# Kernel tuning notes

Hardware: AMD Instinct MI355X
Metric: run time of the kernel (lower is better)

The kernel has to match this reference:

```python
import jax, jax.numpy as jnp
import numpy as np


def setup_inputs() -> dict:
    key = jax.random.key(0)
    ks = jax.random.split(key, 8)
    B, C, H, W = 4, 512, 64, 64
    C8 = C // 8
    return {
        "x": jax.random.normal(ks[0], (B, C, H, W), dtype=jnp.float32),
        "Wq": jax.random.normal(ks[1], (C8, C), dtype=jnp.float32) * 0.02,
        "bq": jax.random.normal(ks[2], (C8,), dtype=jnp.float32) * 0.02,
        "Wk": jax.random.normal(ks[3], (C8, C), dtype=jnp.float32) * 0.02,
        "bk": jax.random.normal(ks[4], (C8,), dtype=jnp.float32) * 0.02,
        "Wv": jax.random.normal(ks[5], (C, C), dtype=jnp.float32) * 0.02,
        "bv": jax.random.normal(ks[6], (C,), dtype=jnp.float32) * 0.02,
        "gamma": jax.random.normal(ks[7], (1,), dtype=jnp.float32),
    }


def reference(x, Wq, bq, Wk, bk, Wv, bv, gamma):
    B, C, H, W = x.shape
    N = H * W
    xf = x.reshape(B, C, N)  # 1x1 conv == per-position matmul over channels
    q = jnp.einsum('oc,bcn->bno', Wq, xf) + bq  # B, N, C//8  (proj_query^T)
    k = jnp.einsum('oc,bcn->bon', Wk, xf) + bk[None, :, None]  # B, C//8, N
    v = jnp.einsum('oc,bcn->bon', Wv, xf) + bv[None, :, None]  # B, C, N
    energy = jnp.einsum('bno,bom->bnm', q, k)  # B, N, N
    attention = jax.nn.softmax(energy, axis=-1)
    # out = bmm(proj_value, attention^T): out[:, :, n] = sum_m v[:, :, m] * att[n, m]
    out = jnp.einsum('bcm,bnm->bcn', v, attention).reshape(B, C, H, W)
    return gamma[0] * out + x
```

## Files before the change

kernel.cpp:

```cpp
#include <hip/hip_runtime.h>
#include <stdint.h>


typedef unsigned short u16;
typedef unsigned char u8;
typedef __attribute__((ext_vector_type(8))) short short8;
typedef __attribute__((ext_vector_type(4))) float f32x4;
typedef __attribute__((ext_vector_type(16))) float f32x16;
typedef __attribute__((ext_vector_type(4))) int i32x4;
typedef __attribute__((ext_vector_type(8))) int i32x8;

#define ASYNC16(gp, lp)                                                        \
  __builtin_amdgcn_global_load_lds(                                            \
      (__attribute__((address_space(1))) void*)(void*)(gp),                    \
      (__attribute__((address_space(3))) void*)(lp), 16, 0, 0)

#define WAIT_VM0 0x0F70
#define WAIT_VM2 0x0F72
#define WAIT_VM4 0x0F74
#define WAIT_VM8 0x0F78

#define EXP_SHIFT 5.0f
#define EXP_CAP 57000.0f

__device__ __forceinline__ u16 f2bf(float f) {
  uint32_t u = __float_as_uint(f);
  u += 0x7FFFu + ((u >> 16) & 1u);
  return (u16)(u >> 16);
}

__device__ __forceinline__ u8 f2fp8(float f) {
  f = fminf(fmaxf(f, -440.f), 440.f);
  int r = __builtin_amdgcn_cvt_pk_fp8_f32(f, f, 0, false);
  return (u8)(r & 0xFF);
}

__global__ __launch_bounds__(256) void k_transpose(const float* __restrict__ x,
                                                   u16* __restrict__ xT) {
  __shared__ float tile[32][33];
  const int b = blockIdx.z;
  const int nb = blockIdx.x * 32;
  const int cb = blockIdx.y * 32;
  const int t = threadIdx.x;
  {
    const int nl = t & 31, c0 = t >> 5;
    const float* xp = x + ((size_t)b * 512 + cb) * 4096 + nb;
#pragma unroll
    for (int i = 0; i < 4; ++i) {
      const int cl = c0 + i * 8;
      tile[cl][nl] = xp[(size_t)cl * 4096 + nl];
    }
  }
  __syncthreads();
  {
    const int cl = t & 31, n0 = t >> 5;
    u16* xtp = xT + ((size_t)b * 4096 + nb) * 512 + cb;
#pragma unroll
    for (int i = 0; i < 4; ++i) {
      const int nl = n0 + i * 8;
      xtp[(size_t)nl * 512 + cl] = f2bf(tile[cl][nl]);
    }
  }
}

__global__ __launch_bounds__(256) void k_wcast(const float* __restrict__ Wq,
                                               const float* __restrict__ Wk,
                                               const float* __restrict__ Wv,
                                               u16* __restrict__ wqk,
                                               u16* __restrict__ wv) {
  const int idx = blockIdx.x * 256 + threadIdx.x;
  if (idx < 128 * 512) {
    const int r = idx >> 9, c = idx & 511;
    const float f = (r < 64) ? Wq[r * 512 + c] : Wk[(r - 64) * 512 + c];
    wqk[idx] = f2bf(f);
  } else {
    const int j = idx - 128 * 512;
    if (j < 512 * 512) wv[j] = f2bf(Wv[j]);
  }
}

__device__ __forceinline__ void gemm_bt_tile(const u16* __restrict__ A,
                                             const u16* __restrict__ B,
                                             const int K, const int rowA0,
                                             const int colB0, u16* smem,
                                             f32x4 acc[4][4]) {
  const int t = threadIdx.x;
  const int lane = t & 63, wave = t >> 6;
  const int quad = lane >> 4, l15 = lane & 15;
  const int wr = wave >> 1, wc = wave & 1;
  u16* As = smem;
  u16* Bs = smem + 8192;
  const f32x4 zero = {0.f, 0.f, 0.f, 0.f};
#pragma unroll
  for (int i = 0; i < 4; ++i)
#pragma unroll
    for (int j = 0; j < 4; ++j) acc[i][j] = zero;

  const int srow = t >> 3;
  const int c8 = (lane & 7) ^ (lane >> 3);
  const u16* ga = A + (size_t)(rowA0 + srow) * K + c8 * 8;
  const u16* gb = B + (size_t)(colB0 + srow) * K + c8 * 8;
  char* la = (char*)As + wave * 1024;
  char* lb = (char*)Bs + wave * 1024;
  const size_t rK32 = (size_t)32 * K;

  const int sw0 = (quad) ^ (l15 & 7);
  const int sw1 = (4 + quad) ^ (l15 & 7);

  for (int k0 = 0; k0 < K; k0 += 64) {
    ASYNC16(ga + k0, la);
    ASYNC16(ga + k0 + rK32, la + 4096);
    ASYNC16(ga + k0 + 2 * rK32, la + 8192);
    ASYNC16(ga + k0 + 3 * rK32, la + 12288);
    ASYNC16(gb + k0, lb);
    ASYNC16(gb + k0 + rK32, lb + 4096);
    ASYNC16(gb + k0 + 2 * rK32, lb + 8192);
    ASYNC16(gb + k0 + 3 * rK32, lb + 12288);
    __syncthreads();
#pragma unroll
    for (int s = 0; s < 2; ++s) {
      const int sw = s ? sw1 : sw0;
      short8 a[4], b[4];
#pragma unroll
      for (int i = 0; i < 4; ++i)
        a[i] = *(const short8*)(As + (wr * 64 + i * 16 + l15) * 64 + sw * 8);
#pragma unroll
      for (int j = 0; j < 4; ++j)
        b[j] = *(const short8*)(Bs + (wc * 64 + j * 16 + l15) * 64 + sw * 8);
#pragma unroll
      for (int i = 0; i < 4; ++i)
#pragma unroll
        for (int j = 0; j < 4; ++j)
          acc[i][j] = __builtin_amdgcn_mfma_f32_16x16x32_bf16(a[i], b[j],
                                                              acc[i][j], 0, 0, 0);
    }
    __syncthreads();
  }
}

__global__ __launch_bounds__(256) void k_proj_qk(const u16* __restrict__ xT,
                                                 const u16* __restrict__ wqk,
                                                 const float* __restrict__ bq,
                                                 const float* __restrict__ bk,
                                                 u16* __restrict__ q,
                                                 u16* __restrict__ kT) {
  __shared__ u16 smem[16384];
  const int b = blockIdx.z;
  const int rowA0 = blockIdx.x * 128;
  f32x4 acc[4][4];
  gemm_bt_tile(xT + (size_t)b * 4096 * 512, wqk, 512, rowA0, 0, smem, acc);
  const int t = threadIdx.x, lane = t & 63, wave = t >> 6;
  const int quad = lane >> 4, l15 = lane & 15;
  const int wr = wave >> 1, wc = wave & 1;
#pragma unroll
  for (int j = 0; j < 4; ++j) {
    const int col = wc * 64 + j * 16 + l15;
    const float bias = (col < 64) ? bq[col] : bk[col - 64];
#pragma unroll
    for (int i = 0; i < 4; ++i) {
#pragma unroll
      for (int r = 0; r < 4; ++r) {
        const int row = rowA0 + wr * 64 + i * 16 + quad * 4 + r;
        const float val = acc[i][j][r] + bias;
        if (col < 64)
          q[((size_t)b * 4096 + row) * 64 + col] = f2bf(val);
        else
          kT[((size_t)b * 4096 + row) * 64 + (col - 64)] = f2bf(val);
      }
    }
  }
}

__global__ __launch_bounds__(256) void k_proj_v(const u16* __restrict__ wv,
                                                const u16* __restrict__ xT,
                                                const float* __restrict__ bv,
                                                u8* __restrict__ v8) {
  __shared__ u16 smem[16384];
  const int b = blockIdx.z;
  const int rowA0 = blockIdx.x * 128;
  const int colB0 = blockIdx.y * 128;
  f32x4 acc[4][4];
  gemm_bt_tile(wv, xT + (size_t)b * 4096 * 512, 512, rowA0, colB0, smem, acc);
  const int t = threadIdx.x, lane = t & 63, wave = t >> 6;
  const int quad = lane >> 4, l15 = lane & 15;
  const int wr = wave >> 1, wc = wave & 1;
#pragma unroll
  for (int i = 0; i < 4; ++i) {
#pragma unroll
    for (int r = 0; r < 4; ++r) {
      const int row = rowA0 + wr * 64 + i * 16 + quad * 4 + r;
      const float bias = bv[row];
#pragma unroll
      for (int j = 0; j < 4; ++j) {
        const int col = colB0 + wc * 64 + j * 16 + l15;
        v8[((size_t)b * 512 + row) * 4096 + col] = f2fp8(acc[i][j][r] + bias);
      }
    }
  }
}

__global__ __launch_bounds__(256, 4) void k_attn(const u16* __restrict__ q,
                                                 const u16* __restrict__ kT,
                                                 u8* __restrict__ E8,
                                                 float* __restrict__ lpart) {
  __shared__ u16 qs[4][16 * 64];
  __shared__ u16 ks[2][128 * 64];

  const int t = threadIdx.x;
  const int l = t & 63;
  const int w = t >> 6;
  const int quad = l >> 4, l15 = l & 15;
  const int c8 = (l & 7) ^ (l >> 3);
  const int r8 = l >> 3;

  const int row0 = blockIdx.x * 64 + w * 16;
  const int mpart = blockIdx.y;
  const int b = blockIdx.z;
  const int m_base = mpart * 1024;

  const u16* qg = q + ((size_t)b * 4096 + row0) * 64 + (size_t)r8 * 64 + c8 * 8;
  const u16* kg = kT + ((size_t)b * 4096 + m_base + w * 32) * 64 +
                  (size_t)r8 * 64 + c8 * 8;

  char* qls = (char*)qs + w * 2048;
  char* kls0 = (char*)ks[0] + w * 4096;
  char* kls1 = (char*)ks[1] + w * 4096;

  ASYNC16(qg, qls);
  ASYNC16(qg + 512, qls + 1024);
#pragma unroll
  for (int i = 0; i < 4; ++i) ASYNC16(kg + i * 512, kls0 + i * 1024);
#pragma unroll
  for (int i = 0; i < 4; ++i) ASYNC16(kg + 8192 + i * 512, kls1 + i * 1024);

  __builtin_amdgcn_s_waitcnt(WAIT_VM8);

  const int sw0 = quad ^ (l15 & 7);
  const int sw1 = (4 + quad) ^ (l15 & 7);
  const u16* qsw = qs[w];
  const short8 af0 = *(const short8*)(qsw + l15 * 64 + sw0 * 8);
  const short8 af1 = *(const short8*)(qsw + l15 * 64 + sw1 * 8);

  float lsum = 0.f;
  u8* Ep = E8 + ((size_t)b * 4096 + row0 + l15) * 4096 + m_base + quad * 4;
  const f32x4 zero = {0.f, 0.f, 0.f, 0.f};

  for (int it = 0; it < 8; ++it) {
    if (it < 7)
      __builtin_amdgcn_s_waitcnt(WAIT_VM4);
    else
      __builtin_amdgcn_s_waitcnt(WAIT_VM0);
    __builtin_amdgcn_s_barrier();
    asm volatile("" ::: "memory");

    const u16* kb = ks[it & 1];
    f32x4 acc[8];
#pragma unroll
    for (int j = 0; j < 8; ++j) acc[j] = zero;
    __builtin_amdgcn_s_setprio(1);
#pragma unroll
    for (int j = 0; j < 8; ++j)
      acc[j] = __builtin_amdgcn_mfma_f32_16x16x32_bf16(
          *(const short8*)(kb + (j * 16 + l15) * 64 + sw0 * 8), af0, acc[j], 0, 0, 0);
#pragma unroll
    for (int j = 0; j < 8; ++j)
      acc[j] = __builtin_amdgcn_mfma_f32_16x16x32_bf16(
          *(const short8*)(kb + (j * 16 + l15) * 64 + sw1 * 8), af1, acc[j], 0, 0, 0);
    __builtin_amdgcn_s_setprio(0);
#pragma unroll
    for (int j = 0; j < 8; ++j) {
      const float e0 = fminf(__expf(acc[j][0] - EXP_SHIFT), EXP_CAP);
      const float e1 = fminf(__expf(acc[j][1] - EXP_SHIFT), EXP_CAP);
      const float e2 = fminf(__expf(acc[j][2] - EXP_SHIFT), EXP_CAP);
      const float e3 = fminf(__expf(acc[j][3] - EXP_SHIFT), EXP_CAP);
      lsum += (e0 + e1) + (e2 + e3);
      int pk = __builtin_amdgcn_cvt_pk_bf8_f32(e0, e1, 0, false);
      pk = __builtin_amdgcn_cvt_pk_bf8_f32(e2, e3, pk, true);
      *(int*)(Ep + it * 128 + j * 16) = pk;
    }

    asm volatile("" ::: "memory");
    __builtin_amdgcn_s_barrier();
    if (it < 6) {
      char* dst = (it & 1) ? kls1 : kls0;
      const u16* src = kg + (size_t)(it + 2) * 8192;
#pragma unroll
      for (int i = 0; i < 4; ++i) ASYNC16(src + i * 512, dst + i * 1024);
    }
  }

  lsum += __shfl_xor(lsum, 16);
  lsum += __shfl_xor(lsum, 32);
  if (l < 16)
    lpart[(size_t)mpart * 16384 + (size_t)b * 4096 + row0 + l] = lsum;
}

__global__ __launch_bounds__(256) void k_lsum(const float* __restrict__ lp,
                                              float* __restrict__ ilg) {
  const int i = blockIdx.x * 256 + threadIdx.x;
  ilg[i] = 1.0f / (lp[i] + lp[16384 + i] + lp[32768 + i] + lp[49152 + i]);
}

__global__ __launch_bounds__(512, 4) void k_pv(const u8* __restrict__ v8,
                                               const u8* __restrict__ E8,
                                               const float* __restrict__ ilg,
                                               const float* __restrict__ x,
                                               const float* __restrict__ gamma,
                                               float* __restrict__ out) {
  __shared__ u8 As[4][8192];
  __shared__ u8 Bs[4][8192];
  const int bid = blockIdx.x;
  const int xcd = bid & 7;
  const int slot = bid >> 3;
  const int c_idx = slot >> 4;
  const int group = xcd * 16 + (slot & 15);
  const int b = group >> 5;
  const int n_idx = group & 31;
  const int rowA0 = c_idx * 128;
  const int colB0 = n_idx * 128;

  const u8* Ag = v8 + (size_t)b * 512 * 4096;
  const u8* Bg = E8 + (size_t)b * 4096 * 4096;

  const int t = threadIdx.x;
  const int l = t & 63, w = t >> 6;
  const int wr = w >> 2, wc = w & 3;
  const int l31 = l & 31, h = l >> 5;

  const int srow = w * 16 + (l >> 2);
  const int ca = l & 3;
  const int fs = (srow >> 1) & 3;
  const u8* gA = Ag + (size_t)(rowA0 + srow) * 4096 + (ca ^ fs) * 16;
  const u8* gB = Bg + (size_t)(colB0 + srow) * 4096 + (ca ^ fs) * 16;

#define STAGE_PV(bi, k0)                                                       \
  do {                                                                         \
    ASYNC16(gA + (k0), (char*)As[bi] + w * 1024);                              \
    ASYNC16(gB + (k0), (char*)Bs[bi] + w * 1024);                              \
  } while (0)

  int rowA[2], sA1[2], sA2[2];
#pragma unroll
  for (int i = 0; i < 2; ++i) {
    rowA[i] = wr * 64 + i * 32 + l31;
    const int fa = (rowA[i] >> 1) & 3;
    sA1[i] = (2 * h) ^ fa;
    sA2[i] = (2 * h + 1) ^ fa;
  }
  const int rowB = wc * 32 + l31;
  const int fb = (rowB >> 1) & 3;
  const int sB1 = (2 * h) ^ fb;
  const int sB2 = (2 * h + 1) ^ fb;

  f32x16 acc[2];
#pragma unroll
  for (int i = 0; i < 2; ++i)
#pragma unroll
    for (int r = 0; r < 16; ++r) acc[i][r] = 0.f;

  STAGE_PV(0, 0);
  STAGE_PV(1, 64);
  STAGE_PV(2, 128);

  for (int it = 0; it < 64; ++it) {
    if (it < 62)
      __builtin_amdgcn_s_waitcnt(WAIT_VM4);
    else if (it == 62)
      __builtin_amdgcn_s_waitcnt(WAIT_VM2);
    else
      __builtin_amdgcn_s_waitcnt(WAIT_VM0);
    asm volatile("" ::: "memory");
    __builtin_amdgcn_s_barrier();
    asm volatile("" ::: "memory");
    if (it + 3 < 64) STAGE_PV((it + 3) & 3, (it + 3) * 64);

    const u8* Asb = As[it & 3];
    const u8* Bsb = Bs[it & 3];
    i32x8 a[2], bb;
#pragma unroll
    for (int i = 0; i < 2; ++i) {
      const u8* pa = Asb + rowA[i] * 64;
      const i32x4 lo = *(const i32x4*)(pa + sA1[i] * 16);
      const i32x4 hi = *(const i32x4*)(pa + sA2[i] * 16);
      a[i][0] = lo[0]; a[i][1] = lo[1]; a[i][2] = lo[2]; a[i][3] = lo[3];
      a[i][4] = hi[0]; a[i][5] = hi[1]; a[i][6] = hi[2]; a[i][7] = hi[3];
    }
    {
      const u8* pb = Bsb + rowB * 64;
      const i32x4 blo = *(const i32x4*)(pb + sB1 * 16);
      const i32x4 bhi = *(const i32x4*)(pb + sB2 * 16);
      bb[0] = blo[0]; bb[1] = blo[1]; bb[2] = blo[2]; bb[3] = blo[3];
      bb[4] = bhi[0]; bb[5] = bhi[1]; bb[6] = bhi[2]; bb[7] = bhi[3];
    }
    __builtin_amdgcn_s_setprio(1);
#pragma unroll
    for (int i = 0; i < 2; ++i)
      acc[i] = __builtin_amdgcn_mfma_scale_f32_32x32x64_f8f6f4(
          a[i], bb, acc[i], 0 , 1 , 0, 0x7F, 0, 0x7F);
    __builtin_amdgcn_s_setprio(0);
    asm volatile("" ::: "memory");
  }
#undef STAGE_PV

  const float g = gamma[0];
  const int col = colB0 + wc * 32 + l31;
  const float gil = g * ilg[(size_t)b * 4096 + col];
#pragma unroll
  for (int i = 0; i < 2; ++i) {
#pragma unroll
    for (int r = 0; r < 16; ++r) {
      const int rloc = (r & 3) + 8 * (r >> 2) + 4 * h;
      const int row = rowA0 + wr * 64 + i * 32 + rloc;
      const size_t idx = ((size_t)b * 512 + row) * 4096 + col;
      out[idx] = gil * acc[i][r] + x[idx];
    }
  }
}

extern "C" void kernel_launch(void* const* d_in, const int* in_sizes, int n_in,
                              void* d_out, int out_size, void* d_ws,
                              size_t ws_size, hipStream_t stream) {
  const float* x = (const float*)d_in[0];
  const float* Wq = (const float*)d_in[1];
  const float* bq = (const float*)d_in[2];
  const float* Wk = (const float*)d_in[3];
  const float* bk = (const float*)d_in[4];
  const float* Wv = (const float*)d_in[5];
  const float* bv = (const float*)d_in[6];
  const float* gamma = (const float*)d_in[7];
  float* out = (float*)d_out;

  char* ws = (char*)d_ws;
  u16* xT = (u16*)(ws);
  u16* wqk = (u16*)(ws + 16777216);
  u16* wv = (u16*)(ws + 16908288);
  u16* qb = (u16*)(ws + 17432576);
  u16* ktb = (u16*)(ws + 19529728);
  u8* v8 = (u8*)(ws + 21626880);
  u8* E8 = (u8*)(ws + 30015488);
  float* lpart = (float*)(ws + 97124352);
  float* ilg = (float*)(ws + 97386496);

  k_transpose<<<dim3(128, 16, 4), 256, 0, stream>>>(x, xT);
  k_wcast<<<dim3(1280), 256, 0, stream>>>(Wq, Wk, Wv, wqk, wv);
  k_proj_qk<<<dim3(32, 1, 4), 256, 0, stream>>>(xT, wqk, bq, bk, qb, ktb);
  k_proj_v<<<dim3(4, 32, 4), 256, 0, stream>>>(wv, xT, bv, v8);
  k_attn<<<dim3(64, 4, 4), 256, 0, stream>>>(qb, ktb, E8, lpart);
  k_lsum<<<dim3(64), 256, 0, stream>>>(lpart, ilg);
  k_pv<<<dim3(512), 512, 0, stream>>>(v8, E8, ilg, x, gamma, out);
}
```

Before: 210.2 us.

## Fuse attention, softmax sum and PV into one flash-style kernel

The separate energy/exp kernel, row-sum kernel and PV GEMM are replaced by one fused kernel. It computes QK^T tiles, exponentiates them into an fp8 P tile in LDS, and accumulates V·P^T directly. This removes the 64MB E8 intermediate write and re-read plus two launches. In exchange, QK^T and exp are recomputed for each of the two channel halves, and the grid is only 256 blocks with a single-stage double buffer that waits for all loads before each step, so overlap and occupancy are reduced.

After: 207.2 us. No clear change (-1.4%).

```diff
diff --git a/kernel.cpp b/kernel.cpp
--- a/kernel.cpp
+++ b/kernel.cpp
@@ -16,9 +16,8 @@
       (__attribute__((address_space(3))) void*)(lp), 16, 0, 0)
 
 #define WAIT_VM0 0x0F70
-#define WAIT_VM2 0x0F72
-#define WAIT_VM4 0x0F74
-#define WAIT_VM8 0x0F78
+#define WAIT_VM6 0x0F76
+#define WAIT_LGKM0 0xC07F
 
 #define EXP_SHIFT 5.0f
 #define EXP_CAP 57000.0f
@@ -199,218 +198,182 @@
   }
 }
 
-__global__ __launch_bounds__(256, 4) void k_attn(const u16* __restrict__ q,
-                                                 const u16* __restrict__ kT,
-                                                 u8* __restrict__ E8,
-                                                 float* __restrict__ lpart) {
-  __shared__ u16 qs[4][16 * 64];
-  __shared__ u16 ks[2][128 * 64];
+__global__ __launch_bounds__(512, 2) void k_fused(const u16* __restrict__ q,
+                                                  const u16* __restrict__ kT,
+                                                  const u8* __restrict__ v8,
+                                                  const float* __restrict__ x,
+                                                  const float* __restrict__ gamma,
+                                                  float* __restrict__ out) {
+  __shared__ u16 k_lds[2][128 * 64];
+  __shared__ u8 v_lds[2][2][256 * 64];
+  __shared__ u8 P_lds[2][128 * 64];
+  __shared__ float lsum_lds[128];
 
   const int t = threadIdx.x;
-  const int l = t & 63;
-  const int w = t >> 6;
+  const int l = t & 63, w = t >> 6;
   const int quad = l >> 4, l15 = l & 15;
-  const int c8 = (l & 7) ^ (l >> 3);
-  const int r8 = l >> 3;
-
-  const int row0 = blockIdx.x * 64 + w * 16;
-  const int mpart = blockIdx.y;
+  const int l31 = l & 31, h = l >> 5;
+
+  const int n0 = blockIdx.x * 128;
+  const int c0 = blockIdx.y * 256;
   const int b = blockIdx.z;
-  const int m_base = mpart * 1024;
-
-  const u16* qg = q + ((size_t)b * 4096 + row0) * 64 + (size_t)r8 * 64 + c8 * 8;
-  const u16* kg = kT + ((size_t)b * 4096 + m_base + w * 32) * 64 +
-                  (size_t)r8 * 64 + c8 * 8;
-
-  char* qls = (char*)qs + w * 2048;
-  char* kls0 = (char*)ks[0] + w * 4096;
-  char* kls1 = (char*)ks[1] + w * 4096;
-
-  ASYNC16(qg, qls);
-  ASYNC16(qg + 512, qls + 1024);
-#pragma unroll
-  for (int i = 0; i < 4; ++i) ASYNC16(kg + i * 512, kls0 + i * 1024);
-#pragma unroll
-  for (int i = 0; i < 4; ++i) ASYNC16(kg + 8192 + i * 512, kls1 + i * 1024);
-
-  __builtin_amdgcn_s_waitcnt(WAIT_VM8);
-
+
+  const u16* qg = q + ((size_t)b * 4096 + n0) * 64;
+  const u16* kg = kT + (size_t)b * 4096 * 64;
+  const u8* vg = v8 + ((size_t)b * 512 + c0) * 4096;
+
+  const int p0 = t, p1 = t + 512;
+  const int kr0 = p0 >> 3, kc0 = p0 & 7;
+  const int kr1 = p1 >> 3, kc1 = p1 & 7;
+  const u16* qs0 = qg + kr0 * 64 + (kc0 ^ (kr0 & 7)) * 8;
+  const u16* qs1 = qg + kr1 * 64 + (kc1 ^ (kr1 & 7)) * 8;
+  const u16* ks0g = kg + kr0 * 64 + (kc0 ^ (kr0 & 7)) * 8;
+  const u16* ks1g = kg + kr1 * 64 + (kc1 ^ (kr1 & 7)) * 8;
+  const int vr0 = p0 >> 2, va0 = p0 & 3;
+  const int vr1 = p1 >> 2, va1 = p1 & 3;
+  const u8* vs0 = vg + (size_t)vr0 * 4096 + (va0 ^ ((vr0 >> 1) & 3)) * 16;
+  const u8* vs1 = vg + (size_t)vr1 * 4096 + (va1 ^ ((vr1 >> 1) & 3)) * 16;
+
+#define STAGE_F(bi, m0)                                                        \
+  do {                                                                         \
+    ASYNC16(ks0g + (m0) * 64, (char*)k_lds[bi] + w * 1024);                    \
+    ASYNC16(ks1g + (m0) * 64, (char*)k_lds[bi] + 8192 + w * 1024);             \
+    ASYNC16(vs0 + (m0), (char*)v_lds[bi][0] + w * 1024);                       \
+    ASYNC16(vs1 + (m0), (char*)v_lds[bi][0] + 8192 + w * 1024);                \
+    ASYNC16(vs0 + (m0) + 64, (char*)v_lds[bi][1] + w * 1024);                  \
+    ASYNC16(vs1 + (m0) + 64, (char*)v_lds[bi][1] + 8192 + w * 1024);           \
+  } while (0)
+
+  ASYNC16(qs0, (char*)P_lds[0] + w * 1024);
+  ASYNC16(qs1, (char*)P_lds[0] + 8192 + w * 1024);
+  STAGE_F(0, 0);
+  __builtin_amdgcn_s_waitcnt(WAIT_VM6);
+  __builtin_amdgcn_s_barrier();
+  asm volatile("" ::: "memory");
   const int sw0 = quad ^ (l15 & 7);
   const int sw1 = (4 + quad) ^ (l15 & 7);
-  const u16* qsw = qs[w];
-  const short8 af0 = *(const short8*)(qsw + l15 * 64 + sw0 * 8);
-  const short8 af1 = *(const short8*)(qsw + l15 * 64 + sw1 * 8);
+  const u16* qrow = (const u16*)P_lds[0] + (w * 16 + l15) * 64;
+  const short8 af0 = *(const short8*)(qrow + sw0 * 8);
+  const short8 af1 = *(const short8*)(qrow + sw1 * 8);
+  asm volatile("" ::: "memory");
+  __builtin_amdgcn_s_waitcnt(WAIT_LGKM0);
+  __builtin_amdgcn_s_barrier();
+  asm volatile("" ::: "memory");
+
+  const int wrp = w >> 2, wcp = w & 3;
+  int rowA[4], sA1[4], sA2[4];
+#pragma unroll
+  for (int i = 0; i < 4; ++i) {
+    rowA[i] = wrp * 128 + i * 32 + l31;
+    const int fa = (rowA[i] >> 1) & 3;
+    sA1[i] = (2 * h) ^ fa;
+    sA2[i] = (2 * h + 1) ^ fa;
+  }
+  const int rowB = wcp * 32 + l31;
+  const int fbB = (rowB >> 1) & 3;
+  const int sB1 = (2 * h) ^ fbB;
+  const int sB2 = (2 * h + 1) ^ fbB;
+
+  const int fbW = (l15 >> 1) & 3;
+  u8* Pw = P_lds[0] + ((w * 16 + l15) * 64) + quad * 4;
+
+  f32x16 acc[4];
+#pragma unroll
+  for (int i = 0; i < 4; ++i)
+#pragma unroll
+    for (int r = 0; r < 16; ++r) acc[i][r] = 0.f;
 
   float lsum = 0.f;
-  u8* Ep = E8 + ((size_t)b * 4096 + row0 + l15) * 4096 + m_base + quad * 4;
   const f32x4 zero = {0.f, 0.f, 0.f, 0.f};
 
-  for (int it = 0; it < 8; ++it) {
-    if (it < 7)
-      __builtin_amdgcn_s_waitcnt(WAIT_VM4);
-    else
-      __builtin_amdgcn_s_waitcnt(WAIT_VM0);
+  for (int it = 0; it < 32; ++it) {
+    __builtin_amdgcn_s_waitcnt(WAIT_VM0);
+    asm volatile("" ::: "memory");
     __builtin_amdgcn_s_barrier();
     asm volatile("" ::: "memory");
-
-    const u16* kb = ks[it & 1];
-    f32x4 acc[8];
-#pragma unroll
-    for (int j = 0; j < 8; ++j) acc[j] = zero;
+    const int cur = it & 1;
+    if (it + 1 < 32) STAGE_F(cur ^ 1, (it + 1) * 128);
+
+    const u16* kb = k_lds[cur];
+    f32x4 eacc[8];
+#pragma unroll
+    for (int j = 0; j < 8; ++j) eacc[j] = zero;
     __builtin_amdgcn_s_setprio(1);
 #pragma unroll
     for (int j = 0; j < 8; ++j)
-      acc[j] = __builtin_amdgcn_mfma_f32_16x16x32_bf16(
-          *(const short8*)(kb + (j * 16 + l15) * 64 + sw0 * 8), af0, acc[j], 0, 0, 0);
+      eacc[j] = __builtin_amdgcn_mfma_f32_16x16x32_bf16(
+          *(const short8*)(kb + (j * 16 + l15) * 64 + sw0 * 8), af0, eacc[j],
+          0, 0, 0);
 #pragma unroll
     for (int j = 0; j < 8; ++j)
-      acc[j] = __builtin_amdgcn_mfma_f32_16x16x32_bf16(
-          *(const short8*)(kb + (j * 16 + l15) * 64 + sw1 * 8), af1, acc[j], 0, 0, 0);
+      eacc[j] = __builtin_amdgcn_mfma_f32_16x16x32_bf16(
+          *(const short8*)(kb + (j * 16 + l15) * 64 + sw1 * 8), af1, eacc[j],
+          0, 0, 0);
     __builtin_amdgcn_s_setprio(0);
+
 #pragma unroll
     for (int j = 0; j < 8; ++j) {
-      const float e0 = fminf(__expf(acc[j][0] - EXP_SHIFT), EXP_CAP);
-      const float e1 = fminf(__expf(acc[j][1] - EXP_SHIFT), EXP_CAP);
-      const float e2 = fminf(__expf(acc[j][2] - EXP_SHIFT), EXP_CAP);
-      const float e3 = fminf(__expf(acc[j][3] - EXP_SHIFT), EXP_CAP);
+      const float e0 = fminf(__expf(eacc[j][0] - EXP_SHIFT), EXP_CAP);
+      const float e1 = fminf(__expf(eacc[j][1] - EXP_SHIFT), EXP_CAP);
+      const float e2 = fminf(__expf(eacc[j][2] - EXP_SHIFT), EXP_CAP);
+      const float e3 = fminf(__expf(eacc[j][3] - EXP_SHIFT), EXP_CAP);
       lsum += (e0 + e1) + (e2 + e3);
       int pk = __builtin_amdgcn_cvt_pk_bf8_f32(e0, e1, 0, false);
       pk = __builtin_amdgcn_cvt_pk_bf8_f32(e2, e3, pk, true);
-      *(int*)(Ep + it * 128 + j * 16) = pk;
-    }
-
+      *(int*)(Pw + (j >> 2) * 8192 + ((j & 3) ^ fbW) * 16) = pk;
+    }
     asm volatile("" ::: "memory");
+    __builtin_amdgcn_s_waitcnt(WAIT_LGKM0);
     __builtin_amdgcn_s_barrier();
-    if (it < 6) {
-      char* dst = (it & 1) ? kls1 : kls0;
-      const u16* src = kg + (size_t)(it + 2) * 8192;
-#pragma unroll
-      for (int i = 0; i < 4; ++i) ASYNC16(src + i * 512, dst + i * 1024);
-    }
-  }
+    asm volatile("" ::: "memory");
+
+#pragma unroll
+    for (int ks = 0; ks < 2; ++ks) {
+      const u8* Vb = v_lds[cur][ks];
+      const u8* Pb = P_lds[ks];
+      i32x8 bb;
+      {
+        const u8* pb = Pb + rowB * 64;
+        const i32x4 blo = *(const i32x4*)(pb + sB1 * 16);
+        const i32x4 bhi = *(const i32x4*)(pb + sB2 * 16);
+        bb[0] = blo[0]; bb[1] = blo[1]; bb[2] = blo[2]; bb[3] = blo[3];
+        bb[4] = bhi[0]; bb[5] = bhi[1]; bb[6] = bhi[2]; bb[7] = bhi[3];
+      }
+      __builtin_amdgcn_s_setprio(1);
+#pragma unroll
+      for (int i = 0; i < 4; ++i) {
+        const u8* pa = Vb + rowA[i] * 64;
+        const i32x4 lo = *(const i32x4*)(pa + sA1[i] * 16);
+        const i32x4 hi = *(const i32x4*)(pa + sA2[i] * 16);
+        i32x8 a;
+        a[0] = lo[0]; a[1] = lo[1]; a[2] = lo[2]; a[3] = lo[3];
+        a[4] = hi[0]; a[5] = hi[1]; a[6] = hi[2]; a[7] = hi[3];
+        acc[i] = __builtin_amdgcn_mfma_scale_f32_32x32x64_f8f6f4(
+            a, bb, acc[i], 0 , 1 , 0, 0x7F, 0, 0x7F);
+      }
+      __builtin_amdgcn_s_setprio(0);
+    }
+    asm volatile("" ::: "memory");
+  }
+#undef STAGE_F
 
   lsum += __shfl_xor(lsum, 16);
   lsum += __shfl_xor(lsum, 32);
-  if (l < 16)
-    lpart[(size_t)mpart * 16384 + (size_t)b * 4096 + row0 + l] = lsum;
-}
-
-__global__ __launch_bounds__(256) void k_lsum(const float* __restrict__ lp,
-                                              float* __restrict__ ilg) {
-  const int i = blockIdx.x * 256 + threadIdx.x;
-  ilg[i] = 1.0f / (lp[i] + lp[16384 + i] + lp[32768 + i] + lp[49152 + i]);
-}
-
-__global__ __launch_bounds__(512, 4) void k_pv(const u8* __restrict__ v8,
-                                               const u8* __restrict__ E8,
-                                               const float* __restrict__ ilg,
-                                               const float* __restrict__ x,
-                                               const float* __restrict__ gamma,
-                                               float* __restrict__ out) {
-  __shared__ u8 As[4][8192];
-  __shared__ u8 Bs[4][8192];
-  const int bid = blockIdx.x;
-  const int xcd = bid & 7;
-  const int slot = bid >> 3;
-  const int c_idx = slot >> 4;
-  const int group = xcd * 16 + (slot & 15);
-  const int b = group >> 5;
-  const int n_idx = group & 31;
-  const int rowA0 = c_idx * 128;
-  const int colB0 = n_idx * 128;
-
-  const u8* Ag = v8 + (size_t)b * 512 * 4096;
-  const u8* Bg = E8 + (size_t)b * 4096 * 4096;
-
-  const int t = threadIdx.x;
-  const int l = t & 63, w = t >> 6;
-  const int wr = w >> 2, wc = w & 3;
-  const int l31 = l & 31, h = l >> 5;
-
-  const int srow = w * 16 + (l >> 2);
-  const int ca = l & 3;
-  const int fs = (srow >> 1) & 3;
-  const u8* gA = Ag + (size_t)(rowA0 + srow) * 4096 + (ca ^ fs) * 16;
-  const u8* gB = Bg + (size_t)(colB0 + srow) * 4096 + (ca ^ fs) * 16;
-
-#define STAGE_PV(bi, k0)                                                       \
-  do {                                                                         \
-    ASYNC16(gA + (k0), (char*)As[bi] + w * 1024);                              \
-    ASYNC16(gB + (k0), (char*)Bs[bi] + w * 1024);                              \
-  } while (0)
-
-  int rowA[2], sA1[2], sA2[2];
-#pragma unroll
-  for (int i = 0; i < 2; ++i) {
-    rowA[i] = wr * 64 + i * 32 + l31;
-    const int fa = (rowA[i] >> 1) & 3;
-    sA1[i] = (2 * h) ^ fa;
-    sA2[i] = (2 * h + 1) ^ fa;
-  }
-  const int rowB = wc * 32 + l31;
-  const int fb = (rowB >> 1) & 3;
-  const int sB1 = (2 * h) ^ fb;
-  const int sB2 = (2 * h + 1) ^ fb;
-
-  f32x16 acc[2];
-#pragma unroll
-  for (int i = 0; i < 2; ++i)
-#pragma unroll
-    for (int r = 0; r < 16; ++r) acc[i][r] = 0.f;
-
-  STAGE_PV(0, 0);
-  STAGE_PV(1, 64);
-  STAGE_PV(2, 128);
-
-  for (int it = 0; it < 64; ++it) {
-    if (it < 62)
-      __builtin_amdgcn_s_waitcnt(WAIT_VM4);
-    else if (it == 62)
-      __builtin_amdgcn_s_waitcnt(WAIT_VM2);
-    else
-      __builtin_amdgcn_s_waitcnt(WAIT_VM0);
-    asm volatile("" ::: "memory");
-    __builtin_amdgcn_s_barrier();
-    asm volatile("" ::: "memory");
-    if (it + 3 < 64) STAGE_PV((it + 3) & 3, (it + 3) * 64);
-
-    const u8* Asb = As[it & 3];
-    const u8* Bsb = Bs[it & 3];
-    i32x8 a[2], bb;
-#pragma unroll
-    for (int i = 0; i < 2; ++i) {
-      const u8* pa = Asb + rowA[i] * 64;
-      const i32x4 lo = *(const i32x4*)(pa + sA1[i] * 16);
-      const i32x4 hi = *(const i32x4*)(pa + sA2[i] * 16);
-      a[i][0] = lo[0]; a[i][1] = lo[1]; a[i][2] = lo[2]; a[i][3] = lo[3];
-      a[i][4] = hi[0]; a[i][5] = hi[1]; a[i][6] = hi[2]; a[i][7] = hi[3];
-    }
-    {
-      const u8* pb = Bsb + rowB * 64;
-      const i32x4 blo = *(const i32x4*)(pb + sB1 * 16);
-      const i32x4 bhi = *(const i32x4*)(pb + sB2 * 16);
-      bb[0] = blo[0]; bb[1] = blo[1]; bb[2] = blo[2]; bb[3] = blo[3];
-      bb[4] = bhi[0]; bb[5] = bhi[1]; bb[6] = bhi[2]; bb[7] = bhi[3];
-    }
-    __builtin_amdgcn_s_setprio(1);
-#pragma unroll
-    for (int i = 0; i < 2; ++i)
-      acc[i] = __builtin_amdgcn_mfma_scale_f32_32x32x64_f8f6f4(
-          a[i], bb, acc[i], 0 , 1 , 0, 0x7F, 0, 0x7F);
-    __builtin_amdgcn_s_setprio(0);
-    asm volatile("" ::: "memory");
-  }
-#undef STAGE_PV
+  if (l < 16) lsum_lds[w * 16 + l15] = lsum;
+  asm volatile("" ::: "memory");
+  __builtin_amdgcn_s_waitcnt(WAIT_LGKM0);
+  __builtin_amdgcn_s_barrier();
+  asm volatile("" ::: "memory");
 
   const float g = gamma[0];
-  const int col = colB0 + wc * 32 + l31;
-  const float gil = g * ilg[(size_t)b * 4096 + col];
-#pragma unroll
-  for (int i = 0; i < 2; ++i) {
+  const int col = n0 + wcp * 32 + l31;
+  const float gil = g / lsum_lds[wcp * 32 + l31];
+#pragma unroll
+  for (int i = 0; i < 4; ++i) {
 #pragma unroll
     for (int r = 0; r < 16; ++r) {
       const int rloc = (r & 3) + 8 * (r >> 2) + 4 * h;
-      const int row = rowA0 + wr * 64 + i * 32 + rloc;
+      const int row = c0 + wrp * 128 + i * 32 + rloc;
       const size_t idx = ((size_t)b * 512 + row) * 4096 + col;
       out[idx] = gil * acc[i][r] + x[idx];
     }
@@ -437,15 +400,10 @@
   u16* qb = (u16*)(ws + 17432576);
   u16* ktb = (u16*)(ws + 19529728);
   u8* v8 = (u8*)(ws + 21626880);
-  u8* E8 = (u8*)(ws + 30015488);
-  float* lpart = (float*)(ws + 97124352);
-  float* ilg = (float*)(ws + 97386496);
 
   k_transpose<<<dim3(128, 16, 4), 256, 0, stream>>>(x, xT);
   k_wcast<<<dim3(1280), 256, 0, stream>>>(Wq, Wk, Wv, wqk, wv);
   k_proj_qk<<<dim3(32, 1, 4), 256, 0, stream>>>(xT, wqk, bq, bk, qb, ktb);
   k_proj_v<<<dim3(4, 32, 4), 256, 0, stream>>>(wv, xT, bv, v8);
-  k_attn<<<dim3(64, 4, 4), 256, 0, stream>>>(qb, ktb, E8, lpart);
-  k_lsum<<<dim3(64), 256, 0, stream>>>(lpart, ilg);
-  k_pv<<<dim3(512), 512, 0, stream>>>(v8, E8, ilg, x, gamma, out);
-}
+  k_fused<<<dim3(32, 2, 4), 512, 0, stream>>>(qb, ktb, v8, x, gamma, out);
+}
```
